# Performance work log

Measured on AMD Instinct MI355X. Metric: run time of the kernel, lower is better.

## Reference

```python
import jax, jax.numpy as jnp
import numpy as np

N_E = 1024
E_DIM = 256
BETA = 0.25


def setup_inputs() -> dict:
    key = jax.random.key(0)
    k1, k2 = jax.random.split(key)
    z = jax.random.normal(k1, (16, 256, 64, 64), dtype=jnp.float32)
    # embedding initialized uniform(-1/n_e, 1/n_e)
    emb = jax.random.uniform(k2, (N_E, E_DIM), dtype=jnp.float32,
                             minval=-1.0 / N_E, maxval=1.0 / N_E)
    return {"z": z, "emb": emb}


def reference(z, emb):
    # z: [B, C, H, W] with C == e_dim; emb: [n_e, e_dim]
    z_perm = jnp.transpose(z, (0, 2, 3, 1))            # [B, H, W, C]
    zf = z_perm.reshape(-1, E_DIM)                      # [N, C]

    # pairwise squared distances: ||z||^2 + ||e||^2 - 2 z e^T  -> [N, n_e]
    d = (jnp.sum(zf * zf, axis=1, keepdims=True)
         + jnp.sum(emb * emb, axis=1)
         - 2.0 * jnp.matmul(zf, emb.T))

    idx = jnp.argmin(d, axis=1)                         # [N]
    zq_flat = emb[idx]                                  # gather [N, C]
    z_q = zq_flat.reshape(z_perm.shape)                 # [B, H, W, C]

    one_hot = jax.nn.one_hot(idx, N_E, dtype=jnp.float32)  # [N, n_e]

    codebook_loss = jnp.mean((jax.lax.stop_gradient(z_q) - z_perm) ** 2)
    commitment_loss = jnp.mean((z_q - jax.lax.stop_gradient(z_perm)) ** 2)
    loss = codebook_loss + BETA * commitment_loss

    # straight-through estimator
    z_q = z_perm + jax.lax.stop_gradient(z_q - z_perm)

    e_mean = jnp.mean(one_hot, axis=0)                  # [n_e]
    perplexity = jnp.exp(-jnp.sum(e_mean * jnp.log(e_mean + 1e-10)))

    z_q = jnp.transpose(z_q, (0, 3, 1, 2))              # [B, C, H, W]
    idx_ret = idx[:, None]
    return (z_q, loss, perplexity, one_hot, idx_ret, d)
```

## Files before the change

kernel.cpp:

```cpp
#include <hip/hip_runtime.h>
#include <math.h>


typedef unsigned short ushort;
typedef unsigned int uint;
typedef __attribute__((ext_vector_type(8))) short  bf16x8;
typedef __attribute__((ext_vector_type(8))) ushort ushort8v;
typedef __attribute__((ext_vector_type(4))) float  f32x4;

static const size_t O_LOSS = 16777216;
static const size_t O_PERP = 16777217;
static const size_t O_OH   = 16777218;
static const size_t O_IDX  = 83886082;
static const size_t O_D    = 83951618;

static const size_t WS_ENORM = 0;
static const size_t WS_ZNF   = 4096;
static const size_t WS_IDX   = 266240;
static const size_t WS_HIST  = 528384;
static const size_t WS_FCNT  = 532480;
static const size_t WS_FROWS = 532496;
static const size_t WS_LOSS  = 794640;
static const size_t WS_AHI   = 9191440;
static const size_t WS_BHI   = 42745872;

#define THR_FLAG 4e-4f

__device__ __forceinline__ ushort f2bf(float f) {
  uint u = __float_as_uint(f);
  return (ushort)((u + 0x7FFFu + ((u >> 16) & 1u)) >> 16);
}
__device__ __forceinline__ void gload16(const void* g, void* l) {
  __builtin_amdgcn_global_load_lds(
      (const __attribute__((address_space(1))) void*)g,
      (__attribute__((address_space(3))) void*)l, 16, 0, 0);
}

__global__ __launch_bounds__(256) void vq_prep_e(const float* __restrict__ emb,
    float* __restrict__ enormf, ushort* __restrict__ Bhi,
    int* __restrict__ hist, int* __restrict__ flag_cnt) {
  const int j = blockIdx.x * 256 + threadIdx.x;
  hist[j] = 0;
  if (j == 0) *flag_cnt = 0;
  const float* e = emb + ((size_t)j << 8);
  ushort* br = Bhi + ((size_t)j << 8);
  double s = 0.0;
  for (int k0 = 0; k0 < 256; k0 += 8) {
    const float4 a = *(const float4*)&e[k0];
    const float4 b = *(const float4*)&e[k0 + 4];
    ushort8v v;
    v[0] = f2bf(a.x); v[1] = f2bf(a.y); v[2] = f2bf(a.z); v[3] = f2bf(a.w);
    v[4] = f2bf(b.x); v[5] = f2bf(b.y); v[6] = f2bf(b.z); v[7] = f2bf(b.w);
    *(ushort8v*)&br[k0] = v;
    s += (double)a.x * (double)a.x;  s += (double)a.y * (double)a.y;
    s += (double)a.z * (double)a.z;  s += (double)a.w * (double)a.w;
    s += (double)b.x * (double)b.x;  s += (double)b.y * (double)b.y;
    s += (double)b.z * (double)b.z;  s += (double)b.w * (double)b.w;
  }
  enormf[j] = (float)s;
}

__global__ __launch_bounds__(256) void vq_prep_z(const float* __restrict__ z,
    ushort* __restrict__ Ahi, float* __restrict__ znf) {
  __shared__ float As[256][68];
  __shared__ double znp[64][4];
  const int t = threadIdx.x;
  const int lane = t & 63, quad = t >> 6;
  const int blk = blockIdx.x;
  const float* zb = z + (((size_t)(blk >> 6)) << 20) + (((size_t)(blk & 63)) << 6);
  {
    const int kr = t >> 4, xc = (t & 15) << 2;
    for (int k0 = 0; k0 < 256; k0 += 16) {
      const int k = k0 + kr;
      *(float4*)&As[k][xc] = *(const float4*)&zb[((size_t)k << 12) + xc];
    }
  }
  __syncthreads();
  {
    double s = 0.0;
    const int kb = quad << 6;
    for (int k = 0; k < 64; ++k) { const double v = (double)As[kb + k][lane]; s += v * v; }
    znp[lane][quad] = s;
  }
  __syncthreads();
  const int m0 = ((blk >> 6) << 12) + ((blk & 63) << 6);
  if (t < 64) znf[m0 + t] = (float)(znp[t][0] + znp[t][1] + znp[t][2] + znp[t][3]);
  const int row = t >> 2;
  const int swz = (row & 7) << 3;
  ushort* dst = Ahi + ((size_t)(m0 + row) << 8);
  for (int s = 0; s < 8; ++s) {
    const int k0 = ((t & 3) + (s << 2)) << 3;
    ushort8v v;
#pragma unroll
    for (int i = 0; i < 8; ++i) v[i] = f2bf(As[k0 + i][row]);
    *(ushort8v*)&dst[k0 ^ swz] = v;
  }
}

__global__ __launch_bounds__(512, 4) void vq_mega(const ushort* __restrict__ Ahi,
    const ushort* __restrict__ Bhi, const float* __restrict__ znf,
    const float* __restrict__ enormf, float* __restrict__ out,
    int* __restrict__ idxw, int* __restrict__ hist,
    int* __restrict__ flag_cnt, int* __restrict__ flag_rows,
    double* __restrict__ loss_part) {
  __shared__ ushort As[32768];
  __shared__ ushort Bs[2][4096];

  const int t = threadIdx.x;
  const int lane = t & 63;
  const int w = t >> 6;
  const int wr = w >> 1;
  const int wc = w & 1;
  const int g = lane >> 4, cl = lane & 15;
  const int m0 = blockIdx.x << 7;
  float* dmat = out + O_D;

  {
    const size_t abase = (size_t)m0 << 8;
    const int off = t << 3;
#pragma unroll
    for (int i = 0; i < 8; ++i)
      gload16(Ahi + abase + (i << 12) + off, &As[(i << 12) + off]);
    gload16(Bhi + ((size_t)(t >> 2) << 8) + ((t & 3) << 3), &Bs[0][t << 3]);
  }

  float zn_[2][4];
#pragma unroll
  for (int ai = 0; ai < 2; ++ai)
#pragma unroll
    for (int rg = 0; rg < 4; ++rg)
      zn_[ai][rg] = znf[m0 + (wr << 5) + (ai << 4) + (g << 2) + rg];

  f32x4 acc[2][4];
#pragma unroll
  for (int a = 0; a < 2; ++a)
#pragma unroll
    for (int b = 0; b < 4; ++b) acc[a][b] = (f32x4)(0.0f);
  float run1[8], run2[8]; int runi[8];
#pragma unroll
  for (int r = 0; r < 8; ++r) { run1[r] = 3.0e38f; run2[r] = 3.0e38f; runi[r] = 0; }

  __syncthreads();

  int cur = 0;
  for (int it = 0; it < 64; ++it) {
    const int nt = it >> 3, kch = it & 7;
    if (it < 63) {
      const int nit = it + 1;
      const int nnt = nit >> 3, nkch = nit & 7;
      gload16(Bhi + ((size_t)(nnt) << 15) + (nkch << 5) +
                  ((size_t)(t >> 2) << 8) + ((t & 3) << 3),
              &Bs[cur ^ 1][t << 3]);
    }
    {
      const int kb = kch << 5;
      bf16x8 av[2], bv[4];
#pragma unroll
      for (int ai = 0; ai < 2; ++ai) {
        const int row = (wr << 5) + (ai << 4) + cl;
        av[ai] = *(const bf16x8*)&As[(row << 8) + ((kb + (g << 3)) ^ ((cl & 7) << 3))];
      }
#pragma unroll
      for (int bj = 0; bj < 4; ++bj)
        bv[bj] = *(const bf16x8*)&Bs[cur][(((wc << 6) + (bj << 4) + cl) << 5) + (g << 3)];
#pragma unroll
      for (int ai = 0; ai < 2; ++ai)
#pragma unroll
        for (int bj = 0; bj < 4; ++bj)
          acc[ai][bj] = __builtin_amdgcn_mfma_f32_16x16x32_bf16(av[ai], bv[bj], acc[ai][bj], 0, 0, 0);
    }
    if (kch == 7) {
      float en_[4];
#pragma unroll
      for (int bj = 0; bj < 4; ++bj)
        en_[bj] = enormf[(nt << 7) + (wc << 6) + (bj << 4) + cl];
#pragma unroll
      for (int ai = 0; ai < 2; ++ai) {
#pragma unroll
        for (int bj = 0; bj < 4; ++bj) {
          const int n = (nt << 7) + (wc << 6) + (bj << 4) + cl;
#pragma unroll
          for (int rg = 0; rg < 4; ++rg) {
            const float S = zn_[ai][rg] + en_[bj];
            const float v = S - 2.0f * acc[ai][bj][rg];
            const int m = m0 + (wr << 5) + (ai << 4) + (g << 2) + rg;
            dmat[((size_t)m << 10) + n] = v;
            const int rr = (ai << 2) + rg;
            if (v < run1[rr]) { run2[rr] = run1[rr]; run1[rr] = v; runi[rr] = n; }
            else if (v < run2[rr]) { run2[rr] = v; }
          }
          acc[ai][bj] = (f32x4)(0.0f);
        }
      }
    }
    __syncthreads();
    cur ^= 1;
  }

  float*  sd1  = (float*)As;
  int*    si1  = (int*)((char*)As + 1024);
  float*  sd2  = (float*)((char*)As + 2048);
  int*    idxs = (int*)((char*)As + 3072);
  double* red  = (double*)((char*)As + 3584);

#pragma unroll
  for (int rr = 0; rr < 8; ++rr) {
    float a1 = run1[rr], a2 = run2[rr]; int ai1 = runi[rr];
    for (int off = 8; off >= 1; off >>= 1) {
      const float o1 = __shfl_xor(a1, off, 16);
      const int   oi = __shfl_xor(ai1, off, 16);
      const float o2 = __shfl_xor(a2, off, 16);
      const float ns = fminf(fminf(a2, o2), fmaxf(a1, o1));
      if (o1 < a1 || (o1 == a1 && oi < ai1)) { a1 = o1; ai1 = oi; }
      a2 = ns;
    }
    if (cl == 0) {
      const int r = (wr << 5) + ((rr >> 2) << 4) + (g << 2) + (rr & 3);
      sd1[(r << 1) + wc] = a1; si1[(r << 1) + wc] = ai1; sd2[(r << 1) + wc] = a2;
    }
  }
  __syncthreads();
  if (t < 128) {
    const float a1 = sd1[t << 1], b1 = sd1[(t << 1) + 1];
    const int ai1 = si1[t << 1], bi1 = si1[(t << 1) + 1];
    const float a2 = sd2[t << 1], b2 = sd2[(t << 1) + 1];
    float d1, d2; int i1;
    if (b1 < a1 || (b1 == a1 && bi1 < ai1)) { d1 = b1; i1 = bi1; d2 = fminf(a1, b2); }
    else { d1 = a1; i1 = ai1; d2 = fminf(b1, a2); }
    const int m = m0 + t;
    idxw[m] = i1; idxs[t] = i1;
    out[O_IDX + m] = (float)i1;
    atomicAdd(&hist[i1], 1);
    if (d2 - d1 < THR_FLAG) {
      const int p = atomicAdd(flag_cnt, 1);
      flag_rows[p] = m;
    }
    red[t] = (double)d1;
  }
  __syncthreads();
  for (int off = 64; off > 0; off >>= 1) {
    if (t < off) red[t] += red[t + off];
    __syncthreads();
  }
  if (t == 0) loss_part[blockIdx.x] = red[0];
  __syncthreads();

  float2* ohbase = (float2*)(out + O_OH);
  for (int rr = 0; rr < 16; ++rr) {
    const int r = (w << 4) + rr;
    const int idx = idxs[r];
    float2* row = ohbase + (((size_t)(m0 + r)) << 9);
    const int half = idx >> 1;
#pragma unroll
    for (int i = 0; i < 8; ++i) {
      const int slot = (i << 6) + lane;
      float2 v; v.x = 0.0f; v.y = 0.0f;
      if (slot == half) { if (idx & 1) v.y = 1.0f; else v.x = 1.0f; }
      row[slot] = v;
    }
  }
}

__global__ __launch_bounds__(256) void vq_refine(const float* __restrict__ z,
    const float* __restrict__ emb, const float* __restrict__ znf,
    const float* __restrict__ enormf, const int* __restrict__ flag_cnt,
    const int* __restrict__ flag_rows, int* __restrict__ idxw,
    float* __restrict__ out, int* __restrict__ hist) {
  __shared__ float zrow[256];
  __shared__ float dmin_s[4];
  __shared__ int cand[256];
  __shared__ int ncand_s;
  __shared__ float rv[256];
  __shared__ int ri[256];
  const float* dmat = out + O_D;
  const int t = threadIdx.x;
  const int n = *flag_cnt;
  for (int f = blockIdx.x; f < n; f += gridDim.x) {
    const int m = flag_rows[f];
    __syncthreads();
    if (t == 0) ncand_s = 0;
    zrow[t] = z[(((size_t)(m >> 12)) << 20) + (size_t)(m & 4095) + ((size_t)t << 12)];
    const float* dr = dmat + ((size_t)m << 10);
    const float2 a = *(const float2*)&dr[t << 2];
    const float2 b = *(const float2*)&dr[(t << 2) + 2];
    float dmin = fminf(fminf(a.x, a.y), fminf(b.x, b.y));
    for (int off = 32; off >= 1; off >>= 1) dmin = fminf(dmin, __shfl_xor(dmin, off));
    if ((t & 63) == 0) dmin_s[t >> 6] = dmin;
    __syncthreads();
    dmin = fminf(fminf(dmin_s[0], dmin_s[1]), fminf(dmin_s[2], dmin_s[3]));
    const float lim = dmin + THR_FLAG;
    const float dv[4] = {a.x, a.y, b.x, b.y};
#pragma unroll
    for (int q = 0; q < 4; ++q)
      if (dv[q] <= lim) {
        const int p = atomicAdd(&ncand_s, 1);
        if (p < 256) cand[p] = (t << 2) + q;
      }
    __syncthreads();
    const int nc = min(ncand_s, 256);
    float best = 3.0e38f; int bi = 1 << 30;
    if (t < nc) {
      const int j = cand[t];
      const float* er = emb + ((size_t)j << 8);
      float s = 0.0f;
      for (int k = 0; k < 256; ++k) s = fmaf(zrow[k], er[k], s);
      const float S = znf[m] + enormf[j];
      best = S - 2.0f * s;
      bi = j;
    }
    rv[t] = best; ri[t] = bi;
    __syncthreads();
    for (int off = 128; off > 0; off >>= 1) {
      if (t < off) {
        const float ov = rv[t + off]; const int oi = ri[t + off];
        if (ov < rv[t] || (ov == rv[t] && oi < ri[t])) { rv[t] = ov; ri[t] = oi; }
      }
      __syncthreads();
    }
    if (t == 0) {
      const int nbi = ri[0];
      const int old = idxw[m];
      if (nbi != old) {
        idxw[m] = nbi;
        out[O_IDX + m] = (float)nbi;
        out[O_OH + ((size_t)m << 10) + (size_t)old] = 0.0f;
        out[O_OH + ((size_t)m << 10) + (size_t)nbi] = 1.0f;
        atomicAdd(&hist[old], -1);
        atomicAdd(&hist[nbi], 1);
      }
    }
  }
}

__global__ __launch_bounds__(256) void vq_zq(const float* __restrict__ emb,
    const int* __restrict__ idxw, float* __restrict__ zq) {
  __shared__ float E[64][258];
  __shared__ int il[64];
  const int t = threadIdx.x;
  const int blk = blockIdx.x;
  const int base = blk << 6;
  if (t < 64) il[t] = idxw[base + t];
  __syncthreads();
  for (int i = 0; i < 64; ++i) E[i][t] = emb[((size_t)il[i] << 8) + t];
  __syncthreads();
  const int w = t & 63, cg = t >> 6;
  const size_t zbase = (((size_t)(blk >> 6)) << 20) + (((size_t)(blk & 63)) << 6) + (size_t)w;
  for (int ci = 0; ci < 64; ++ci) {
    const int c = (ci << 2) + cg;
    zq[zbase + ((size_t)c << 12)] = E[w][c];
  }
}

__global__ __launch_bounds__(256) void vq_final(const double* __restrict__ loss_part,
    const int* __restrict__ hist, float* __restrict__ out) {
  __shared__ double red[256];
  const int t = threadIdx.x;
  red[t] = loss_part[t] + loss_part[t + 256];
  __syncthreads();
  for (int off = 128; off > 0; off >>= 1) {
    if (t < off) red[t] += red[t + off];
    __syncthreads();
  }
  if (t == 0) out[O_LOSS] = (float)(1.25 * red[0] / 16777216.0);
  __syncthreads();
  double h = 0.0;
  for (int i = t; i < 1024; i += 256) {
    const double p = (double)hist[i] / 65536.0;
    h += p * log(p + 1e-10);
  }
  red[t] = h;
  __syncthreads();
  for (int off = 128; off > 0; off >>= 1) {
    if (t < off) red[t] += red[t + off];
    __syncthreads();
  }
  if (t == 0) out[O_PERP] = (float)exp(-red[0]);
}

extern "C" void kernel_launch(void* const* d_in, const int* in_sizes, int n_in,
                              void* d_out, int out_size, void* d_ws, size_t ws_size,
                              hipStream_t stream) {
  const float* z   = (const float*)d_in[0];
  const float* emb = (const float*)d_in[1];
  float* out = (float*)d_out;
  char* ws = (char*)d_ws;

  float*  enormf    = (float*)(ws + WS_ENORM);
  float*  znf       = (float*)(ws + WS_ZNF);
  int*    idxw      = (int*)(ws + WS_IDX);
  int*    hist      = (int*)(ws + WS_HIST);
  int*    flag_cnt  = (int*)(ws + WS_FCNT);
  int*    flag_rows = (int*)(ws + WS_FROWS);
  double* loss_part = (double*)(ws + WS_LOSS);
  ushort* Ahi       = (ushort*)(ws + WS_AHI);
  ushort* Bhi       = (ushort*)(ws + WS_BHI);

  vq_prep_e<<<4, 256, 0, stream>>>(emb, enormf, Bhi, hist, flag_cnt);
  vq_prep_z<<<1024, 256, 0, stream>>>(z, Ahi, znf);
  vq_mega<<<512, 512, 0, stream>>>(Ahi, Bhi, znf, enormf, out, idxw, hist,
                                   flag_cnt, flag_rows, loss_part);
  vq_refine<<<4096, 256, 0, stream>>>(z, emb, znf, enormf, flag_cnt, flag_rows,
                                      idxw, out, hist);
  vq_zq<<<1024, 256, 0, stream>>>(emb, idxw, out);
  vq_final<<<1, 256, 0, stream>>>(loss_part, hist, out);
}
```

Baseline: 326.6 us.

## Fuse z preprocessing and z_q gather into the main distance kernel

Removes the separate z-prep kernel and its bf16 workspace. The main kernel now loads z directly, transposes it through shared memory, converts it to bf16 and computes row norms. It also drops the separate z_q gather kernel: the main kernel writes z_q from the argmin indices, and the refine kernel rewrites the z_q column for any row whose index changes. This saves two launches and the round trip of the A matrix through global memory. In exchange it adds a serial prologue before the MFMA loop and an extra write phase at the end.

```diff
diff --git a/kernel.cpp b/kernel.cpp
--- a/kernel.cpp
+++ b/kernel.cpp
@@ -21,8 +21,7 @@
 static const size_t WS_FCNT  = 532480;
 static const size_t WS_FROWS = 532496;
 static const size_t WS_LOSS  = 794640;
-static const size_t WS_AHI   = 9191440;
-static const size_t WS_BHI   = 42745872;
+static const size_t WS_BHI   = 798736;
 
 #define THR_FLAG 4e-4f
 
@@ -60,48 +59,11 @@
   enormf[j] = (float)s;
 }
 
-__global__ __launch_bounds__(256) void vq_prep_z(const float* __restrict__ z,
-    ushort* __restrict__ Ahi, float* __restrict__ znf) {
-  __shared__ float As[256][68];
-  __shared__ double znp[64][4];
-  const int t = threadIdx.x;
-  const int lane = t & 63, quad = t >> 6;
-  const int blk = blockIdx.x;
-  const float* zb = z + (((size_t)(blk >> 6)) << 20) + (((size_t)(blk & 63)) << 6);
-  {
-    const int kr = t >> 4, xc = (t & 15) << 2;
-    for (int k0 = 0; k0 < 256; k0 += 16) {
-      const int k = k0 + kr;
-      *(float4*)&As[k][xc] = *(const float4*)&zb[((size_t)k << 12) + xc];
-    }
-  }
-  __syncthreads();
-  {
-    double s = 0.0;
-    const int kb = quad << 6;
-    for (int k = 0; k < 64; ++k) { const double v = (double)As[kb + k][lane]; s += v * v; }
-    znp[lane][quad] = s;
-  }
-  __syncthreads();
-  const int m0 = ((blk >> 6) << 12) + ((blk & 63) << 6);
-  if (t < 64) znf[m0 + t] = (float)(znp[t][0] + znp[t][1] + znp[t][2] + znp[t][3]);
-  const int row = t >> 2;
-  const int swz = (row & 7) << 3;
-  ushort* dst = Ahi + ((size_t)(m0 + row) << 8);
-  for (int s = 0; s < 8; ++s) {
-    const int k0 = ((t & 3) + (s << 2)) << 3;
-    ushort8v v;
-#pragma unroll
-    for (int i = 0; i < 8; ++i) v[i] = f2bf(As[k0 + i][row]);
-    *(ushort8v*)&dst[k0 ^ swz] = v;
-  }
-}
-
-__global__ __launch_bounds__(512, 4) void vq_mega(const ushort* __restrict__ Ahi,
-    const ushort* __restrict__ Bhi, const float* __restrict__ znf,
+__global__ __launch_bounds__(512, 4) void vq_mega(const float* __restrict__ z,
+    const float* __restrict__ emb, const ushort* __restrict__ Bhi,
     const float* __restrict__ enormf, float* __restrict__ out,
-    int* __restrict__ idxw, int* __restrict__ hist,
-    int* __restrict__ flag_cnt, int* __restrict__ flag_rows,
+    int* __restrict__ idxw, float* __restrict__ znf,
+    int* __restrict__ hist, int* __restrict__ flag_cnt, int* __restrict__ flag_rows,
     double* __restrict__ loss_part) {
   __shared__ ushort As[32768];
   __shared__ ushort Bs[2][4096];
@@ -109,27 +71,56 @@
   const int t = threadIdx.x;
   const int lane = t & 63;
   const int w = t >> 6;
-  const int wr = w >> 1;
-  const int wc = w & 1;
+  const int wr = w >> 1, wc = w & 1;
   const int g = lane >> 4, cl = lane & 15;
-  const int m0 = blockIdx.x << 7;
+  const int blk = blockIdx.x;
+  const int m0 = blk << 7;
+  const int zb = blk >> 5;
+  const int r0 = (blk & 31) << 7;
   float* dmat = out + O_D;
 
+  float* Fs = (float*)&Bs[0][0];
+  const int kk = t >> 5, rq = t & 31;
+  const int arow = t >> 2, gq = t & 3;
+  const int swzr = (arow & 7) << 3;
+  double zn2 = 0.0;
+  for (int kc = 0; kc < 256; kc += 32) {
+    const float4 v0 = *(const float4*)&z[((size_t)zb << 20) + ((size_t)(kc + kk) << 12) + r0 + (rq << 2)];
+    const float4 v1 = *(const float4*)&z[((size_t)zb << 20) + ((size_t)(kc + kk + 16) << 12) + r0 + (rq << 2)];
+    if (kc) __syncthreads();
+    *(float4*)&Fs[(kk << 7) + (rq << 2)] = v0;
+    *(float4*)&Fs[((kk + 16) << 7) + (rq << 2)] = v1;
+    __syncthreads();
+    ushort8v pk;
+#pragma unroll
+    for (int j = 0; j < 8; ++j) {
+      const float v = Fs[(((gq << 3) + j) << 7) | arow];
+      zn2 += (double)v * (double)v;
+      pk[j] = f2bf(v);
+    }
+    *(ushort8v*)&As[(arow << 8) + ((kc + (gq << 3)) ^ swzr)] = pk;
+  }
+  __syncthreads();
   {
-    const size_t abase = (size_t)m0 << 8;
-    const int off = t << 3;
-#pragma unroll
-    for (int i = 0; i < 8; ++i)
-      gload16(Ahi + abase + (i << 12) + off, &As[(i << 12) + off]);
-    gload16(Bhi + ((size_t)(t >> 2) << 8) + ((t & 3) << 3), &Bs[0][t << 3]);
-  }
-
+    double* znp = (double*)&Bs[0][0];
+    znp[(arow << 2) + gq] = zn2;
+  }
+  __syncthreads();
+  float* znf_s = (float*)((char*)&Bs[0][0] + 8192);
+  if (t < 128) {
+    const double* zp = (const double*)&Bs[0][0] + (t << 2);
+    const float zf = (float)(zp[0] + zp[1] + zp[2] + zp[3]);
+    znf[m0 + t] = zf;
+    znf_s[t] = zf;
+  }
+  __syncthreads();
   float zn_[2][4];
 #pragma unroll
   for (int ai = 0; ai < 2; ++ai)
 #pragma unroll
     for (int rg = 0; rg < 4; ++rg)
-      zn_[ai][rg] = znf[m0 + (wr << 5) + (ai << 4) + (g << 2) + rg];
+      zn_[ai][rg] = znf_s[(wr << 5) + (ai << 4) + (g << 2) + rg];
+  gload16(Bhi + ((size_t)(t >> 2) << 8) + ((t & 3) << 3), &Bs[0][t << 3]);
 
   f32x4 acc[2][4];
 #pragma unroll
@@ -147,8 +138,7 @@
     const int nt = it >> 3, kch = it & 7;
     if (it < 63) {
       const int nit = it + 1;
-      const int nnt = nit >> 3, nkch = nit & 7;
-      gload16(Bhi + ((size_t)(nnt) << 15) + (nkch << 5) +
+      gload16(Bhi + ((size_t)(nit >> 3) << 15) + ((nit & 7) << 5) +
                   ((size_t)(t >> 2) << 8) + ((t & 3) << 3),
               &Bs[cur ^ 1][t << 3]);
     }
@@ -197,11 +187,11 @@
     cur ^= 1;
   }
 
-  float*  sd1  = (float*)As;
-  int*    si1  = (int*)((char*)As + 1024);
-  float*  sd2  = (float*)((char*)As + 2048);
-  int*    idxs = (int*)((char*)As + 3072);
-  double* red  = (double*)((char*)As + 3584);
+  float*  sd1  = (float*)&Bs[0][0];
+  int*    si1  = (int*)((char*)&Bs[0][0] + 1024);
+  float*  sd2  = (float*)((char*)&Bs[0][0] + 2048);
+  int*    idxs = (int*)((char*)&Bs[0][0] + 3072);
+  double* red  = (double*)((char*)&Bs[0][0] + 3584);
 
 #pragma unroll
   for (int rr = 0; rr < 8; ++rr) {
@@ -242,8 +232,7 @@
     if (t < off) red[t] += red[t + off];
     __syncthreads();
   }
-  if (t == 0) loss_part[blockIdx.x] = red[0];
-  __syncthreads();
+  if (t == 0) loss_part[blk] = red[0];
 
   float2* ohbase = (float2*)(out + O_OH);
   for (int rr = 0; rr < 16; ++rr) {
@@ -257,6 +246,34 @@
       float2 v; v.x = 0.0f; v.y = 0.0f;
       if (slot == half) { if (idx & 1) v.y = 1.0f; else v.x = 1.0f; }
       row[slot] = v;
+    }
+  }
+
+  float* Et = (float*)As;
+  for (int ch = 0; ch < 4; ++ch) {
+    __syncthreads();
+    {
+      const int e = idxs[arow];
+#pragma unroll
+      for (int j2 = 0; j2 < 4; ++j2) {
+        const int cb = (gq << 4) + (j2 << 2);
+        const float4 ev = *(const float4*)&emb[((size_t)e << 8) + (ch << 6) + cb];
+        Et[(cb + 0) * 132 + arow] = ev.x;
+        Et[(cb + 1) * 132 + arow] = ev.y;
+        Et[(cb + 2) * 132 + arow] = ev.z;
+        Et[(cb + 3) * 132 + arow] = ev.w;
+      }
+    }
+    __syncthreads();
+#pragma unroll
+    for (int i = 0; i < 8; ++i) {
+      const int cll = (w << 3) + i;
+      const int c = (ch << 6) + cll;
+#pragma unroll
+      for (int h = 0; h < 2; ++h) {
+        const int rr = (h << 6) + lane;
+        out[((size_t)zb << 20) + ((size_t)c << 12) + r0 + rr] = Et[cll * 132 + rr];
+      }
     }
   }
 }
@@ -270,6 +287,7 @@
   __shared__ float dmin_s[4];
   __shared__ int cand[256];
   __shared__ int ncand_s;
+  __shared__ int old_s;
   __shared__ float rv[256];
   __shared__ int ri[256];
   const float* dmat = out + O_D;
@@ -278,7 +296,7 @@
   for (int f = blockIdx.x; f < n; f += gridDim.x) {
     const int m = flag_rows[f];
     __syncthreads();
-    if (t == 0) ncand_s = 0;
+    if (t == 0) { ncand_s = 0; old_s = idxw[m]; }
     zrow[t] = z[(((size_t)(m >> 12)) << 20) + (size_t)(m & 4095) + ((size_t)t << 12)];
     const float* dr = dmat + ((size_t)m << 10);
     const float2 a = *(const float2*)&dr[t << 2];
@@ -317,10 +335,10 @@
       }
       __syncthreads();
     }
-    if (t == 0) {
-      const int nbi = ri[0];
-      const int old = idxw[m];
-      if (nbi != old) {
+    const int nbi = ri[0];
+    const int old = old_s;
+    if (nbi != old) {
+      if (t == 0) {
         idxw[m] = nbi;
         out[O_IDX + m] = (float)nbi;
         out[O_OH + ((size_t)m << 10) + (size_t)old] = 0.0f;
@@ -328,26 +346,9 @@
         atomicAdd(&hist[old], -1);
         atomicAdd(&hist[nbi], 1);
       }
-    }
-  }
-}
-
-__global__ __launch_bounds__(256) void vq_zq(const float* __restrict__ emb,
-    const int* __restrict__ idxw, float* __restrict__ zq) {
-  __shared__ float E[64][258];
-  __shared__ int il[64];
-  const int t = threadIdx.x;
-  const int blk = blockIdx.x;
-  const int base = blk << 6;
-  if (t < 64) il[t] = idxw[base + t];
-  __syncthreads();
-  for (int i = 0; i < 64; ++i) E[i][t] = emb[((size_t)il[i] << 8) + t];
-  __syncthreads();
-  const int w = t & 63, cg = t >> 6;
-  const size_t zbase = (((size_t)(blk >> 6)) << 20) + (((size_t)(blk & 63)) << 6) + (size_t)w;
-  for (int ci = 0; ci < 64; ++ci) {
-    const int c = (ci << 2) + cg;
-    zq[zbase + ((size_t)c << 12)] = E[w][c];
+      out[(((size_t)(m >> 12)) << 20) + ((size_t)t << 12) + (size_t)(m & 4095)] =
+          emb[((size_t)nbi << 8) + t];
+    }
   }
 }
 
@@ -392,15 +393,12 @@
   int*    flag_cnt  = (int*)(ws + WS_FCNT);
   int*    flag_rows = (int*)(ws + WS_FROWS);
   double* loss_part = (double*)(ws + WS_LOSS);
-  ushort* Ahi       = (ushort*)(ws + WS_AHI);
   ushort* Bhi       = (ushort*)(ws + WS_BHI);
 
   vq_prep_e<<<4, 256, 0, stream>>>(emb, enormf, Bhi, hist, flag_cnt);
-  vq_prep_z<<<1024, 256, 0, stream>>>(z, Ahi, znf);
-  vq_mega<<<512, 512, 0, stream>>>(Ahi, Bhi, znf, enormf, out, idxw, hist,
+  vq_mega<<<512, 512, 0, stream>>>(z, emb, Bhi, enormf, out, idxw, znf, hist,
                                    flag_cnt, flag_rows, loss_part);
   vq_refine<<<4096, 256, 0, stream>>>(z, emb, znf, enormf, flag_cnt, flag_rows,
                                       idxw, out, hist);
-  vq_zq<<<1024, 256, 0, stream>>>(emb, idxw, out);
   vq_final<<<1, 256, 0, stream>>>(loss_part, hist, out);
 }
```

Measured after the change: 334.2 us. 1.02x slower.
